# Kernel tuning notes

Measured on AMD Instinct MI355X. Metric: run time of the kernel, lower is better.

Reference implementation:

```python
import jax, jax.numpy as jnp
import numpy as np

HW_SCALE = 64.0
B = 1048576  # batch of image pairs


def _forward_once(img, W_conv, W_linear):
    # img: (8, 8). Extract TL, TR, BL, BR 4x4 patches, each flattened to 16.
    # reshape->transpose gives quadrants in row-major order: TL, TR, BL, BR.
    patches = img.reshape(2, 4, 2, 4).transpose(0, 2, 1, 3).reshape(4, 16)
    acc1 = jax.nn.relu(patches @ W_conv)  # (4, 4)
    conv_out = jnp.clip(acc1 / HW_SCALE, -128.0, 127.0)
    # The original scalar double-loop writes conv_out row-major into row 0 of a
    # (4,16) zero matrix; rows 1-3 are zero, so the second matmul reduces to:
    acc2 = conv_out.reshape(16) @ W_linear  # (4,)
    return jnp.clip(acc2 / HW_SCALE, -128.0, 127.0)


def setup_inputs() -> dict:
    key = jax.random.key(0)
    k1, k2, k3, k4 = jax.random.split(key, 4)
    img1 = jax.random.normal(k1, (B, 8, 8), dtype=jnp.float32)
    img2 = jax.random.normal(k2, (B, 8, 8), dtype=jnp.float32)
    W_conv = jax.random.normal(k3, (16, 4), dtype=jnp.float32) * 0.1
    W_linear = jax.random.normal(k4, (16, 4), dtype=jnp.float32) * 0.1
    return {"img1": img1, "img2": img2, "W_conv": W_conv, "W_linear": W_linear}


def reference(img1, img2, W_conv, W_linear):
    f = jax.vmap(_forward_once, in_axes=(0, None, None))
    return f(img1, W_conv, W_linear), f(img2, W_conv, W_linear)
```

## Files before the change

### kernel.cpp

```cpp
#include <hip/hip_runtime.h>


__global__ __launch_bounds__(256) void surrogate_kernel(
    const float* __restrict__ img1, const float* __restrict__ img2,
    const float* __restrict__ Wc,
    const float* __restrict__ Wl,
    float* __restrict__ out,
    int B)
{
    __shared__ float4 tile[256 * 16];

    const int t = threadIdx.x;
    const int blocksPerInput = B >> 8;
    int bid = (int)blockIdx.x;
    const int second = bid >= blocksPerInput ? 1 : 0;
    if (second) bid -= blocksPerInput;
    const float4* src4 = (const float4*)(second ? img2 : img1) + (size_t)bid * 4096;

    float4 r[16];
#pragma unroll
    for (int k = 0; k < 16; ++k) r[k] = src4[k * 256 + t];

    const int q   = t >> 4;
    const int cth = t & 15;
#pragma unroll
    for (int k = 0; k < 16; ++k) {
        const int img = 16 * k + q;
        tile[img * 16 + (cth ^ q)] = r[k];
    }
    __syncthreads();

    const float4* wc4 = (const float4*)Wc;
    const float4* wl4 = (const float4*)Wl;

    float a1[4][4];
#pragma unroll
    for (int p = 0; p < 4; ++p)
#pragma unroll
        for (int c = 0; c < 4; ++c) a1[p][c] = 0.0f;

    const int key = t & 15;
    const int base = t * 16;
#pragma unroll
    for (int c = 0; c < 16; ++c) {
        const float4 v = tile[base + (c ^ key)];
        const int row = c >> 1;
        const int p   = ((row >> 2) << 1) | (c & 1);
        const int rr  = row & 3;
        const float4 w0 = wc4[rr * 4 + 0];
        const float4 w1 = wc4[rr * 4 + 1];
        const float4 w2 = wc4[rr * 4 + 2];
        const float4 w3 = wc4[rr * 4 + 3];
        a1[p][0] = fmaf(v.x, w0.x, a1[p][0]);
        a1[p][1] = fmaf(v.x, w0.y, a1[p][1]);
        a1[p][2] = fmaf(v.x, w0.z, a1[p][2]);
        a1[p][3] = fmaf(v.x, w0.w, a1[p][3]);
        a1[p][0] = fmaf(v.y, w1.x, a1[p][0]);
        a1[p][1] = fmaf(v.y, w1.y, a1[p][1]);
        a1[p][2] = fmaf(v.y, w1.z, a1[p][2]);
        a1[p][3] = fmaf(v.y, w1.w, a1[p][3]);
        a1[p][0] = fmaf(v.z, w2.x, a1[p][0]);
        a1[p][1] = fmaf(v.z, w2.y, a1[p][1]);
        a1[p][2] = fmaf(v.z, w2.z, a1[p][2]);
        a1[p][3] = fmaf(v.z, w2.w, a1[p][3]);
        a1[p][0] = fmaf(v.w, w3.x, a1[p][0]);
        a1[p][1] = fmaf(v.w, w3.y, a1[p][1]);
        a1[p][2] = fmaf(v.w, w3.z, a1[p][2]);
        a1[p][3] = fmaf(v.w, w3.w, a1[p][3]);
    }

    float co[16];
#pragma unroll
    for (int p = 0; p < 4; ++p)
#pragma unroll
        for (int c = 0; c < 4; ++c) {
            float tv = fmaxf(a1[p][c], 0.0f) * 0.015625f;
            co[p * 4 + c] = fminf(fmaxf(tv, -128.0f), 127.0f);
        }

    float a2[4] = {0.0f, 0.0f, 0.0f, 0.0f};
#pragma unroll
    for (int j = 0; j < 16; ++j) {
        const float4 w = wl4[j];
        a2[0] = fmaf(co[j], w.x, a2[0]);
        a2[1] = fmaf(co[j], w.y, a2[1]);
        a2[2] = fmaf(co[j], w.z, a2[2]);
        a2[3] = fmaf(co[j], w.w, a2[3]);
    }

    float4 o;
    o.x = fminf(fmaxf(a2[0] * 0.015625f, -128.0f), 127.0f);
    o.y = fminf(fmaxf(a2[1] * 0.015625f, -128.0f), 127.0f);
    o.z = fminf(fmaxf(a2[2] * 0.015625f, -128.0f), 127.0f);
    o.w = fminf(fmaxf(a2[3] * 0.015625f, -128.0f), 127.0f);
    ((float4*)out)[(size_t)second * B + (size_t)bid * 256 + t] = o;
}

extern "C" void kernel_launch(void* const* d_in, const int* in_sizes, int n_in,
                              void* d_out, int out_size, void* d_ws, size_t ws_size,
                              hipStream_t stream) {
    const float* img1 = (const float*)d_in[0];
    const float* img2 = (const float*)d_in[1];
    const float* Wc   = (const float*)d_in[2];
    const float* Wl   = (const float*)d_in[3];
    float* out = (float*)d_out;

    const int B = in_sizes[0] / 64;
    const int blocks = 2 * (B >> 8);
    hipLaunchKernelGGL(surrogate_kernel, dim3(blocks), dim3(256), 0, stream,
                       img1, img2, Wc, Wl, out, B);
}
```

Baseline: 517.4 us.

## Split each image across four lanes with shuffle reduction and grid-stride loop

Drops the shared-memory transpose tile and instead assigns each 4x4 patch of an image to one of four lanes. Each lane reads its patch directly from global memory and computes its partial linear output, and the partials are combined with xor shuffles. The launch becomes a persistent grid-stride loop capped at 2048 blocks, with a launch-bounds occupancy hint. The aim is to remove LDS traffic, the block barrier and register pressure. In exchange, each lane's global loads are strided float4 accesses rather than fully contiguous ones, and only one lane in four performs the store.

```diff
diff --git a/kernel.cpp b/kernel.cpp
--- a/kernel.cpp
+++ b/kernel.cpp
@@ -1,99 +1,87 @@
 #include <hip/hip_runtime.h>
 
 
-__global__ __launch_bounds__(256) void surrogate_kernel(
+__global__ __launch_bounds__(256, 4) void surrogate_kernel(
     const float* __restrict__ img1, const float* __restrict__ img2,
     const float* __restrict__ Wc,
     const float* __restrict__ Wl,
     float* __restrict__ out,
     int B)
 {
-    __shared__ float4 tile[256 * 16];
-
-    const int t = threadIdx.x;
-    const int blocksPerInput = B >> 8;
-    int bid = (int)blockIdx.x;
-    const int second = bid >= blocksPerInput ? 1 : 0;
-    if (second) bid -= blocksPerInput;
-    const float4* src4 = (const float4*)(second ? img2 : img1) + (size_t)bid * 4096;
-
-    float4 r[16];
-#pragma unroll
-    for (int k = 0; k < 16; ++k) r[k] = src4[k * 256 + t];
-
-    const int q   = t >> 4;
-    const int cth = t & 15;
-#pragma unroll
-    for (int k = 0; k < 16; ++k) {
-        const int img = 16 * k + q;
-        tile[img * 16 + (cth ^ q)] = r[k];
-    }
-    __syncthreads();
+    const int lane = threadIdx.x & 63;
+    const int p    = lane & 3;
+    const int mloc = lane >> 2;
 
     const float4* wc4 = (const float4*)Wc;
     const float4* wl4 = (const float4*)Wl;
 
-    float a1[4][4];
+    const float4 wl0 = wl4[p * 4 + 0];
+    const float4 wl1 = wl4[p * 4 + 1];
+    const float4 wl2 = wl4[p * 4 + 2];
+    const float4 wl3 = wl4[p * 4 + 3];
+
+    const int wavesPerBlock = blockDim.x >> 6;
+    const int waveId = (int)blockIdx.x * wavesPerBlock + ((int)threadIdx.x >> 6);
+    const int nWaves = (int)gridDim.x * wavesPerBlock;
+    const int total  = 2 * B;
+    const int cb     = (p & 1) + ((p >> 1) << 3);
+
+    for (int g0 = waveId << 4; g0 < total; g0 += nWaves << 4) {
+        const int g = g0 + mloc;
+        const float4* s4 = (g0 < B)
+            ? ((const float4*)img1 + ((size_t)g << 4))
+            : ((const float4*)img2 + ((size_t)(g - B) << 4));
+
+        float4 v[4];
+        v[0] = s4[cb + 0];
+        v[1] = s4[cb + 2];
+        v[2] = s4[cb + 4];
+        v[3] = s4[cb + 6];
+
+        float4 a = make_float4(0.f, 0.f, 0.f, 0.f);
 #pragma unroll
-    for (int p = 0; p < 4; ++p)
-#pragma unroll
-        for (int c = 0; c < 4; ++c) a1[p][c] = 0.0f;
-
-    const int key = t & 15;
-    const int base = t * 16;
-#pragma unroll
-    for (int c = 0; c < 16; ++c) {
-        const float4 v = tile[base + (c ^ key)];
-        const int row = c >> 1;
-        const int p   = ((row >> 2) << 1) | (c & 1);
-        const int rr  = row & 3;
-        const float4 w0 = wc4[rr * 4 + 0];
-        const float4 w1 = wc4[rr * 4 + 1];
-        const float4 w2 = wc4[rr * 4 + 2];
-        const float4 w3 = wc4[rr * 4 + 3];
-        a1[p][0] = fmaf(v.x, w0.x, a1[p][0]);
-        a1[p][1] = fmaf(v.x, w0.y, a1[p][1]);
-        a1[p][2] = fmaf(v.x, w0.z, a1[p][2]);
-        a1[p][3] = fmaf(v.x, w0.w, a1[p][3]);
-        a1[p][0] = fmaf(v.y, w1.x, a1[p][0]);
-        a1[p][1] = fmaf(v.y, w1.y, a1[p][1]);
-        a1[p][2] = fmaf(v.y, w1.z, a1[p][2]);
-        a1[p][3] = fmaf(v.y, w1.w, a1[p][3]);
-        a1[p][0] = fmaf(v.z, w2.x, a1[p][0]);
-        a1[p][1] = fmaf(v.z, w2.y, a1[p][1]);
-        a1[p][2] = fmaf(v.z, w2.z, a1[p][2]);
-        a1[p][3] = fmaf(v.z, w2.w, a1[p][3]);
-        a1[p][0] = fmaf(v.w, w3.x, a1[p][0]);
-        a1[p][1] = fmaf(v.w, w3.y, a1[p][1]);
-        a1[p][2] = fmaf(v.w, w3.z, a1[p][2]);
-        a1[p][3] = fmaf(v.w, w3.w, a1[p][3]);
-    }
-
-    float co[16];
-#pragma unroll
-    for (int p = 0; p < 4; ++p)
-#pragma unroll
-        for (int c = 0; c < 4; ++c) {
-            float tv = fmaxf(a1[p][c], 0.0f) * 0.015625f;
-            co[p * 4 + c] = fminf(fmaxf(tv, -128.0f), 127.0f);
+        for (int j = 0; j < 4; ++j) {
+            const float4 vv = v[j];
+            const float4 w0 = wc4[4 * j + 0];
+            const float4 w1 = wc4[4 * j + 1];
+            const float4 w2 = wc4[4 * j + 2];
+            const float4 w3 = wc4[4 * j + 3];
+            a.x = fmaf(vv.x, w0.x, a.x); a.y = fmaf(vv.x, w0.y, a.y);
+            a.z = fmaf(vv.x, w0.z, a.z); a.w = fmaf(vv.x, w0.w, a.w);
+            a.x = fmaf(vv.y, w1.x, a.x); a.y = fmaf(vv.y, w1.y, a.y);
+            a.z = fmaf(vv.y, w1.z, a.z); a.w = fmaf(vv.y, w1.w, a.w);
+            a.x = fmaf(vv.z, w2.x, a.x); a.y = fmaf(vv.z, w2.y, a.y);
+            a.z = fmaf(vv.z, w2.z, a.z); a.w = fmaf(vv.z, w2.w, a.w);
+            a.x = fmaf(vv.w, w3.x, a.x); a.y = fmaf(vv.w, w3.y, a.y);
+            a.z = fmaf(vv.w, w3.z, a.z); a.w = fmaf(vv.w, w3.w, a.w);
         }
 
-    float a2[4] = {0.0f, 0.0f, 0.0f, 0.0f};
-#pragma unroll
-    for (int j = 0; j < 16; ++j) {
-        const float4 w = wl4[j];
-        a2[0] = fmaf(co[j], w.x, a2[0]);
-        a2[1] = fmaf(co[j], w.y, a2[1]);
-        a2[2] = fmaf(co[j], w.z, a2[2]);
-        a2[3] = fmaf(co[j], w.w, a2[3]);
+        float4 co;
+        co.x = fminf(fmaxf(fmaxf(a.x, 0.f) * 0.015625f, -128.f), 127.f);
+        co.y = fminf(fmaxf(fmaxf(a.y, 0.f) * 0.015625f, -128.f), 127.f);
+        co.z = fminf(fmaxf(fmaxf(a.z, 0.f) * 0.015625f, -128.f), 127.f);
+        co.w = fminf(fmaxf(fmaxf(a.w, 0.f) * 0.015625f, -128.f), 127.f);
+
+        float4 t;
+        t.x = fmaf(co.x, wl0.x, fmaf(co.y, wl1.x, fmaf(co.z, wl2.x, co.w * wl3.x)));
+        t.y = fmaf(co.x, wl0.y, fmaf(co.y, wl1.y, fmaf(co.z, wl2.y, co.w * wl3.y)));
+        t.z = fmaf(co.x, wl0.z, fmaf(co.y, wl1.z, fmaf(co.z, wl2.z, co.w * wl3.z)));
+        t.w = fmaf(co.x, wl0.w, fmaf(co.y, wl1.w, fmaf(co.z, wl2.w, co.w * wl3.w)));
+
+        t.x += __shfl_xor(t.x, 1); t.y += __shfl_xor(t.y, 1);
+        t.z += __shfl_xor(t.z, 1); t.w += __shfl_xor(t.w, 1);
+        t.x += __shfl_xor(t.x, 2); t.y += __shfl_xor(t.y, 2);
+        t.z += __shfl_xor(t.z, 2); t.w += __shfl_xor(t.w, 2);
+
+        if (p == 0) {
+            float4 o;
+            o.x = fminf(fmaxf(t.x * 0.015625f, -128.f), 127.f);
+            o.y = fminf(fmaxf(t.y * 0.015625f, -128.f), 127.f);
+            o.z = fminf(fmaxf(t.z * 0.015625f, -128.f), 127.f);
+            o.w = fminf(fmaxf(t.w * 0.015625f, -128.f), 127.f);
+            ((float4*)out)[g] = o;
+        }
     }
-
-    float4 o;
-    o.x = fminf(fmaxf(a2[0] * 0.015625f, -128.0f), 127.0f);
-    o.y = fminf(fmaxf(a2[1] * 0.015625f, -128.0f), 127.0f);
-    o.z = fminf(fmaxf(a2[2] * 0.015625f, -128.0f), 127.0f);
-    o.w = fminf(fmaxf(a2[3] * 0.015625f, -128.0f), 127.0f);
-    ((float4*)out)[(size_t)second * B + (size_t)bid * 256 + t] = o;
 }
 
 extern "C" void kernel_launch(void* const* d_in, const int* in_sizes, int n_in,
@@ -106,7 +94,8 @@
     float* out = (float*)d_out;
 
     const int B = in_sizes[0] / 64;
-    const int blocks = 2 * (B >> 8);
+    int blocks = (2 * B + 63) / 64;
+    if (blocks > 2048) blocks = 2048;
     hipLaunchKernelGGL(surrogate_kernel, dim3(blocks), dim3(256), 0, stream,
                        img1, img2, Wc, Wl, out, B);
 }
```

After: 520.0 us. Within noise of the previous version (+0.5%).
